# Performance work log

Hardware: AMD Instinct MI355X
Metric: run time of the kernel (lower is better)

The kernel has to match this reference:

```python
import jax, jax.numpy as jnp
import numpy as np

V, B, T, D, H = 32000, 64, 256, 512, 1024


def setup_inputs() -> dict:
    key = jax.random.key(0)
    ks = jax.random.split(key, 8)
    s = lambda i, shape: (jax.random.normal(ks[i], shape, jnp.float32) * 0.02)
    return {
        "y": jax.random.randint(ks[0], (B, T), 0, V),
        "hidden": jnp.zeros((B, H), jnp.float32),
        "emb_table": s(1, (V, D)),
        "Wx": s(2, (D, 3 * H)),
        "Wh": s(3, (H, 3 * H)),
        "bx": jnp.zeros((3 * H,), jnp.float32),
        "bh": jnp.zeros((3 * H,), jnp.float32),
        "W_out": s(4, (H, D)),
        "b_out": jnp.zeros((D,), jnp.float32),
    }


def _gru_step(h, x, Wx, Wh, bx, bh):
    # PyTorch GRUCell semantics: r,z gates, candidate n with r gating the
    # recurrent contribution (including its bias term).
    gx = x @ Wx + bx          # [B, 3H]
    gh = h @ Wh + bh          # [B, 3H]
    xr, xz, xn = jnp.split(gx, 3, axis=-1)
    hr, hz, hn = jnp.split(gh, 3, axis=-1)
    r = jax.nn.sigmoid(xr + hr)
    z = jax.nn.sigmoid(xz + hz)
    n = jnp.tanh(xn + r * hn)
    return (1.0 - z) * n + z * h


def reference(y, hidden, emb_table, Wx, Wh, bx, bh, W_out, b_out):
    emb = emb_table[y]                       # [B, T, D] token embedding lookup

    def step(h, x_t):                        # x_t: [B, D]
        h2 = _gru_step(h, x_t, Wx, Wh, bx, bh)
        return h2, h2

    _, outs = jax.lax.scan(step, hidden, jnp.swapaxes(emb, 0, 1))  # [T, B, H]
    out = jnp.swapaxes(outs, 0, 1)           # [B, T, H] decoder hiddens
    logits = jnp.tanh(out @ W_out + b_out)   # [B, T, D]; dropout_rate=0 -> identity
    return logits
```

## Files before the change

### kernel.cpp

```cpp
#include <hip/hip_runtime.h>
#include <stdint.h>

typedef unsigned short u16;
typedef unsigned int u32;
typedef __attribute__((ext_vector_type(4))) unsigned int u32x4;
typedef __attribute__((ext_vector_type(4))) float f32x4;
typedef __attribute__((ext_vector_type(8))) __bf16 bf16x8;

#define MFMA16(a, b, c) __builtin_amdgcn_mfma_f32_16x16x32_bf16((a), (b), (c), 0, 0, 0)

__device__ __forceinline__ u16 f2b(float f) {
  union { float f; unsigned u; } v; v.f = f;
  unsigned r = v.u + 0x7FFFu + ((v.u >> 16) & 1u);
  return (u16)(r >> 16);
}
__device__ __forceinline__ float b2f(u16 h) {
  union { unsigned u; float f; } v; v.u = ((unsigned)h) << 16;
  return v.f;
}
__device__ __forceinline__ float sigm(float x) { return 1.0f / (1.0f + __expf(-x)); }
__device__ __forceinline__ float tanh_fast(float x) {
  x = fminf(fmaxf(x, -15.0f), 15.0f);
  float t = __expf(2.0f * x);
  return (t - 1.0f) / (t + 1.0f);
}

template <int OFF>
__device__ __forceinline__ u32x4 ld16_sc(const void* p) {
  u32x4 r;
  asm volatile("global_load_dwordx4 %0, %1, off offset:%2 sc0 sc1"
               : "=v"(r) : "v"(p), "i"(OFF));
  return r;
}
__device__ __forceinline__ void st16_sc(void* p, u32x4 v) {
  asm volatile("global_store_dwordx4 %0, %1, off sc0 sc1"
               :: "v"(p), "v"(v) : "memory");
}
__device__ __forceinline__ void st4_sc(u32* p, u32 v) {
  asm volatile("global_store_dword %0, %1, off sc0 sc1"
               :: "v"(p), "v"(v) : "memory");
}
__device__ __forceinline__ u32 ld4_sc(const u32* p) {
  u32 r;
  asm volatile("global_load_dword %0, %1, off sc0 sc1\n\t"
               "s_waitcnt vmcnt(0)"
               : "=v"(r) : "v"(p) : "memory");
  return r;
}

__device__ __forceinline__ void gld_lds16(const void* g, void* l) {
  __builtin_amdgcn_global_load_lds(
      (const __attribute__((address_space(1))) void*)(g),
      (__attribute__((address_space(3))) void*)(l), 16, 0, 0);
}

__global__ __launch_bounds__(256) void prep_all(
    const float* __restrict__ Wx, const float* __restrict__ Wh,
    const float* __restrict__ Wout, const int* __restrict__ y,
    const float* __restrict__ emb, const float* __restrict__ hidden,
    u16* __restrict__ wx_t, u16* __restrict__ wh_t, u16* __restrict__ wo_t,
    u16* __restrict__ aemb, u16* __restrict__ hbuf, u32* __restrict__ tags) {
  __shared__ float tile[32][33];
  const int b = blockIdx.x, tid = threadIdx.x;
  const int tx = tid & 31, ty = tid >> 5;

  const float* src = nullptr; u16* dst = nullptr; int R = 0, C = 0, tb = 0;
  if (b < 1536)      { src = Wx;   dst = wx_t; R = 512;  C = 3072; tb = b; }
  else if (b < 4608) { src = Wh;   dst = wh_t; R = 1024; C = 3072; tb = b - 1536; }
  else if (b < 5120) { src = Wout; dst = wo_t; R = 1024; C = 512;  tb = b - 4608; }

  if (src) {
    const int xt = C >> 5;
    const int c0 = (tb % xt) * 32, r0 = (tb / xt) * 32;
    for (int i = ty; i < 32; i += 8)
      tile[i][tx] = src[(size_t)(r0 + i) * C + (c0 + tx)];
    __syncthreads();
    for (int i = ty; i < 32; i += 8)
      dst[(size_t)(c0 + i) * R + (r0 + tx)] = f2b(tile[tx][i]);
    return;
  }
  if (b < 13312) {
    const int idx = (b - 5120) * 256 + tid;
    const int m = idx >> 7, d0 = (idx & 127) << 2;
    const float4 v = *reinterpret_cast<const float4*>(emb + (size_t)y[m] * 512 + d0);
    ushort4 o;
    o.x = f2b(v.x); o.y = f2b(v.y); o.z = f2b(v.z); o.w = f2b(v.w);
    *reinterpret_cast<ushort4*>(aemb + (size_t)m * 512 + d0) = o;
    return;
  }
  if (b < 13568) {
    const int i = (b - 13312) * 256 + tid;
    const int bb = i >> 10, n = i & 1023;
    const int r = bb >> 4, ii = bb & 15, g = n >> 4, j = n & 15;
    hbuf[((size_t)r * 64 + g) * 256 + ii * 16 + j] = f2b(hidden[(size_t)bb * 1024 + n]);
    return;
  }
  {
    const int base = ((b - 13568) * 256 + tid) * 8;
#pragma unroll
    for (int q = 0; q < 8; ++q) tags[base + q] = 0;
  }
}

template <int EPI, int ALAYOUT>
__global__ __launch_bounds__(256, 2) void gemm_bt(
    const u16* __restrict__ A, const u16* __restrict__ Bt,
    const float* __restrict__ bias, void* __restrict__ Cout,
    int M, int N, int K) {
  __shared__ u16 As[4096], Bs[4096];
  const int tid = threadIdx.x, lane = tid & 63, w = tid >> 6;
  const int wm = w >> 1, wn = w & 1, c = lane & 15, hq = lane >> 4;
  const int m0 = blockIdx.y * 128, n0 = blockIdx.x * 128;
  f32x4 acc[4][4] = {};

  const int r0_ = tid >> 2, ko0 = (tid & 3) << 3;
  const int r1_ = (256 + tid) >> 2, ko1 = ((256 + tid) & 3) << 3;

  for (int k0 = 0; k0 < K; k0 += 32) {
    const u16 *ga0, *ga1;
    if (ALAYOUT == 0) {
      ga0 = A + (size_t)(m0 + r0_) * K + k0 + ko0;
      ga1 = A + (size_t)(m0 + r1_) * K + k0 + ko1;
    } else {
      const int ma = m0 + r0_, ka = k0 + ko0, mb = m0 + r1_, kb = k0 + ko1;
      ga0 = A + ((((size_t)(ma >> 6) + 1) * 4 + ((ma >> 4) & 3)) * 64 +
                 (ka >> 4)) * 256 + (ma & 15) * 16 + (ka & 15);
      ga1 = A + ((((size_t)(mb >> 6) + 1) * 4 + ((mb >> 4) & 3)) * 64 +
                 (kb >> 4)) * 256 + (mb & 15) * 16 + (kb & 15);
    }
    const u16* gb0 = Bt + (size_t)(n0 + r0_) * K + k0 + ko0;
    const u16* gb1 = Bt + (size_t)(n0 + r1_) * K + k0 + ko1;
    __syncthreads();
    gld_lds16(ga0, (char*)As + tid * 16);
    gld_lds16(ga1, (char*)As + 4096 + tid * 16);
    gld_lds16(gb0, (char*)Bs + tid * 16);
    gld_lds16(gb1, (char*)Bs + 4096 + tid * 16);
    __syncthreads();
    u32x4 af[4], bf[4];
#pragma unroll
    for (int i = 0; i < 4; ++i) {
      af[i] = *(const u32x4*)(As + (wm * 64 + i * 16 + c) * 32 + hq * 8);
      bf[i] = *(const u32x4*)(Bs + (wn * 64 + i * 16 + c) * 32 + hq * 8);
    }
#pragma unroll
    for (int mi = 0; mi < 4; ++mi)
#pragma unroll
      for (int ni = 0; ni < 4; ++ni)
        acc[mi][ni] = MFMA16(__builtin_bit_cast(bf16x8, af[mi]),
                             __builtin_bit_cast(bf16x8, bf[ni]), acc[mi][ni]);
  }

#pragma unroll
  for (int ni = 0; ni < 4; ++ni) {
    const int col = n0 + wn * 64 + ni * 16 + c;
    const float bv = bias[col];
#pragma unroll
    for (int mi = 0; mi < 4; ++mi) {
#pragma unroll
      for (int i = 0; i < 4; ++i) {
        const int m = m0 + wm * 64 + mi * 16 + hq * 4 + i;
        const float v = acc[mi][ni][i] + bv;
        if (EPI == 0) {
          const int dr = (m & 255) * 64 + (m >> 8);
          ((u16*)Cout)[(size_t)dr * N + col] = f2b(v);
        } else {
          const int dr = (m & 63) * 256 + (m >> 6);
          ((float*)Cout)[(size_t)dr * N + col] = tanh_fast(v);
        }
      }
    }
  }
}

__global__ __launch_bounds__(320, 1) void scan_kernel(
    const u16* __restrict__ wh_t,
    const float* __restrict__ bh,
    const float* __restrict__ h0,
    const u16* __restrict__ gx,
    u16* __restrict__ hbuf,
    u32* __restrict__ tags) {
  __shared__ u16 whs[96 * 512];
  __shared__ float red[2][4][3][256];
  __shared__ __align__(16) u16 htile[16][16];
  const int g = blockIdx.x >> 2, r = blockIdx.x & 3;
  const int tid = threadIdx.x, lane = tid & 63, s = tid >> 6;
  const int c = lane & 15, hq = lane >> 4;
  const int gcol = g * 16 + c;
  const int row0 = r * 16;

  for (int fb = s; fb < 96; fb += 5) {
    const int ss = fb / 24, kk = (fb % 24) / 3, ct = fb % 3;
    const int n = ct * 1024 + g * 16 + c;
    const int k = ss * 256 + kk * 32 + hq * 8;
    *(u32x4*)(whs + fb * 512 + lane * 8) =
        *(const u32x4*)(wh_t + (size_t)n * 1024 + k);
  }
  float bhv[3], hprev[4];
  u16 gxr[4][3];
  if (s == 4) {
#pragma unroll
    for (int ct = 0; ct < 3; ++ct) bhv[ct] = bh[ct * 1024 + gcol];
#pragma unroll
    for (int i = 0; i < 4; ++i)
      hprev[i] = h0[(size_t)(row0 + hq * 4 + i) * 1024 + gcol];
    const u16* gp = gx + gcol;
#pragma unroll
    for (int i = 0; i < 4; ++i) {
      const int b = row0 + hq * 4 + i;
      gxr[i][0] = gp[(size_t)b * 3072];
      gxr[i][1] = gp[(size_t)b * 3072 + 1024];
      gxr[i][2] = gp[(size_t)b * 3072 + 2048];
    }
  }
  __syncthreads();

  for (int t = 0; t < 256; ++t) {
    if (s < 4) {
      if (t > 0 && lane < 16) {
        const u32* tp = tags + (((size_t)(t & 1) * 4 + r) * 64 + s * 16 + lane) * 32;
        while (__ballot(ld4_sc(tp) < (u32)t)) {}
      }

      u32x4 af[8];
      {
        const u16* ap0 = hbuf + ((size_t)t * 4 + r) * 16384 +
                         (s * 16 + (hq >> 1)) * 256 + c * 16 + (hq & 1) * 8;
        const u16* ap1 = ap0 + 2048;
        af[0] = ld16_sc<0>(ap0);    af[1] = ld16_sc<1024>(ap0);
        af[2] = ld16_sc<2048>(ap0); af[3] = ld16_sc<3072>(ap0);
        af[4] = ld16_sc<0>(ap1);    af[5] = ld16_sc<1024>(ap1);
        af[6] = ld16_sc<2048>(ap1); af[7] = ld16_sc<3072>(ap1);
      }
      asm volatile("s_waitcnt vmcnt(0)" ::: "memory");
      __builtin_amdgcn_sched_barrier(0);

      f32x4 acc[3] = {};
#pragma unroll
      for (int kk = 0; kk < 8; ++kk) {
        const int fb = (s * 8 + kk) * 3;
        const u32x4 b0 = *(const u32x4*)(whs + (fb + 0) * 512 + lane * 8);
        const u32x4 b1 = *(const u32x4*)(whs + (fb + 1) * 512 + lane * 8);
        const u32x4 b2 = *(const u32x4*)(whs + (fb + 2) * 512 + lane * 8);
        const bf16x8 a = __builtin_bit_cast(bf16x8, af[kk]);
        acc[0] = MFMA16(a, __builtin_bit_cast(bf16x8, b0), acc[0]);
        acc[1] = MFMA16(a, __builtin_bit_cast(bf16x8, b1), acc[1]);
        acc[2] = MFMA16(a, __builtin_bit_cast(bf16x8, b2), acc[2]);
      }
#pragma unroll
      for (int ct = 0; ct < 3; ++ct)
        *(f32x4*)&red[t & 1][s][ct][lane * 4] = acc[ct];
    }
    __syncthreads();

    if (s == 4) {
      f32x4 a0 = {}, a1 = {}, a2 = {};
#pragma unroll
      for (int j = 0; j < 4; ++j) {
        a0 += *(const f32x4*)&red[t & 1][j][0][lane * 4];
        a1 += *(const f32x4*)&red[t & 1][j][1][lane * 4];
        a2 += *(const f32x4*)&red[t & 1][j][2][lane * 4];
      }
#pragma unroll
      for (int i = 0; i < 4; ++i) {
        const float xr = b2f(gxr[i][0]);
        const float xz = b2f(gxr[i][1]);
        const float xn = b2f(gxr[i][2]);
        const float rr = sigm(xr + a0[i] + bhv[0]);
        const float zz = sigm(xz + a1[i] + bhv[1]);
        const float nn = tanh_fast(xn + rr * (a2[i] + bhv[2]));
        const float hnew = (1.0f - zz) * nn + zz * hprev[i];
        hprev[i] = hnew;
        htile[hq * 4 + i][c] = f2b(hnew);
      }
      asm volatile("s_waitcnt lgkmcnt(0)" ::: "memory");
      __builtin_amdgcn_sched_barrier(0);
      if (lane < 32) {
        const u32x4 hv = *(const u32x4*)((const u16*)htile + lane * 8);
        st16_sc(hbuf + ((size_t)(t + 1) * 4 + r) * 16384 + g * 256 + lane * 8, hv);
      }
      asm volatile("s_waitcnt vmcnt(0)" ::: "memory");
      if (lane == 0)
        st4_sc(tags + (((size_t)((t + 1) & 1) * 4 + r) * 64 + g) * 32, (u32)(t + 1));
      if (t < 255) {
        const u16* gp = gx + (size_t)(t + 1) * 64 * 3072 + gcol;
#pragma unroll
        for (int i = 0; i < 4; ++i) {
          const int b = row0 + hq * 4 + i;
          gxr[i][0] = gp[(size_t)b * 3072];
          gxr[i][1] = gp[(size_t)b * 3072 + 1024];
          gxr[i][2] = gp[(size_t)b * 3072 + 2048];
        }
      }
    }
  }
}

extern "C" void kernel_launch(void* const* d_in, const int* in_sizes, int n_in,
                              void* d_out, int out_size, void* d_ws, size_t ws_size,
                              hipStream_t stream) {
  (void)in_sizes; (void)n_in; (void)out_size; (void)ws_size;
  const int* y = (const int*)d_in[0];
  const float* hidden = (const float*)d_in[1];
  const float* emb = (const float*)d_in[2];
  const float* Wx = (const float*)d_in[3];
  const float* Wh = (const float*)d_in[4];
  const float* bx = (const float*)d_in[5];
  const float* bh = (const float*)d_in[6];
  const float* Wout = (const float*)d_in[7];
  const float* bout = (const float*)d_in[8];

  char* p = (char*)d_ws;
  u16* wx_t = (u16*)p; p += (size_t)3072 * 512 * 2;
  u16* wh_t = (u16*)p; p += (size_t)3072 * 1024 * 2;
  u16* wo_t = (u16*)p; p += (size_t)512 * 1024 * 2;
  u16* aemb = (u16*)p; p += (size_t)16384 * 512 * 2;
  u16* gx   = (u16*)p; p += (size_t)16384 * 3072 * 2;
  u16* hbuf = (u16*)p; p += (size_t)257 * 4 * 64 * 256 * 2;
  u32* tags = (u32*)p;

  prep_all<<<dim3(13600), dim3(256), 0, stream>>>(Wx, Wh, Wout, y, emb, hidden,
                                                  wx_t, wh_t, wo_t, aemb, hbuf,
                                                  tags);
  gemm_bt<0, 0><<<dim3(24, 128), dim3(256), 0, stream>>>(aemb, wx_t, bx, (void*)gx,
                                                         16384, 3072, 512);
  scan_kernel<<<dim3(256), dim3(320), 0, stream>>>(wh_t, bh, hidden, gx,
                                                   hbuf, tags);
  gemm_bt<1, 1><<<dim3(4, 128), dim3(256), 0, stream>>>(hbuf, wo_t, bout,
                                                        d_out, 16384, 512, 1024);
}
```

Baseline: 876.9 us.

## Replace tag-based inter-block sync with in-band flag bits in hidden-state data

Removes the separate tag array and its store-after-wait handshake. The low mantissa bit of every even bf16 element in the hidden-state buffer now serves as a ready flag. The buffer is zeroed beforehand, consumers poll one element per producer and then re-verify every loaded fragment's flag bits, retrying if any are unset. This cuts a global store, a full vmcnt wait and a separate polling round-trip from each recurrent step's critical path. In exchange it perturbs the LSB of half the hidden values, costs extra zeroing of the whole hbuf in prep, and relies on 16-byte stores becoming visible atomically or on the retry loop covering torn writes.

```diff
diff --git a/kernel.cpp b/kernel.cpp
--- a/kernel.cpp
+++ b/kernel.cpp
@@ -36,17 +36,6 @@
   asm volatile("global_store_dwordx4 %0, %1, off sc0 sc1"
                :: "v"(p), "v"(v) : "memory");
 }
-__device__ __forceinline__ void st4_sc(u32* p, u32 v) {
-  asm volatile("global_store_dword %0, %1, off sc0 sc1"
-               :: "v"(p), "v"(v) : "memory");
-}
-__device__ __forceinline__ u32 ld4_sc(const u32* p) {
-  u32 r;
-  asm volatile("global_load_dword %0, %1, off sc0 sc1\n\t"
-               "s_waitcnt vmcnt(0)"
-               : "=v"(r) : "v"(p) : "memory");
-  return r;
-}
 
 __device__ __forceinline__ void gld_lds16(const void* g, void* l) {
   __builtin_amdgcn_global_load_lds(
@@ -59,7 +48,7 @@
     const float* __restrict__ Wout, const int* __restrict__ y,
     const float* __restrict__ emb, const float* __restrict__ hidden,
     u16* __restrict__ wx_t, u16* __restrict__ wh_t, u16* __restrict__ wo_t,
-    u16* __restrict__ aemb, u16* __restrict__ hbuf, u32* __restrict__ tags) {
+    u16* __restrict__ aemb, u16* __restrict__ hbuf) {
   __shared__ float tile[32][33];
   const int b = blockIdx.x, tid = threadIdx.x;
   const int tx = tid & 31, ty = tid >> 5;
@@ -92,13 +81,15 @@
     const int i = (b - 13312) * 256 + tid;
     const int bb = i >> 10, n = i & 1023;
     const int r = bb >> 4, ii = bb & 15, g = n >> 4, j = n & 15;
-    hbuf[((size_t)r * 64 + g) * 256 + ii * 16 + j] = f2b(hidden[(size_t)bb * 1024 + n]);
+    u16 v = f2b(hidden[(size_t)bb * 1024 + n]);
+    if (!(j & 1)) v |= 1;
+    hbuf[((size_t)r * 64 + g) * 256 + ii * 16 + j] = v;
     return;
   }
   {
-    const int base = ((b - 13568) * 256 + tid) * 8;
-#pragma unroll
-    for (int q = 0; q < 8; ++q) tags[base + q] = 0;
+    const size_t idx = (size_t)(b - 13568) * 256 + tid;
+    u32x4 z = {0, 0, 0, 0};
+    *(u32x4*)(hbuf + 65536 + idx * 8) = z;
   }
 }
 
@@ -177,8 +168,7 @@
     const float* __restrict__ bh,
     const float* __restrict__ h0,
     const u16* __restrict__ gx,
-    u16* __restrict__ hbuf,
-    u32* __restrict__ tags) {
+    u16* __restrict__ hbuf) {
   __shared__ u16 whs[96 * 512];
   __shared__ float red[2][4][3][256];
   __shared__ __align__(16) u16 htile[16][16];
@@ -216,23 +206,42 @@
 
   for (int t = 0; t < 256; ++t) {
     if (s < 4) {
-      if (t > 0 && lane < 16) {
-        const u32* tp = tags + (((size_t)(t & 1) * 4 + r) * 64 + s * 16 + lane) * 32;
-        while (__ballot(ld4_sc(tp) < (u32)t)) {}
+      const u16* slotBase = hbuf + ((size_t)t * 4 + r) * 16384;
+
+      if (t > 0) {
+        const u16* pp = slotBase + (s * 16 + (lane & 15)) * 256;
+        u32 v0, v1;
+        if (lane < 16) {
+          asm volatile("global_load_ushort %0, %1, off sc0 sc1" : "=v"(v0) : "v"(pp));
+          asm volatile("global_load_ushort %0, %1, off sc0 sc1" : "=v"(v1) : "v"(pp));
+          while (true) {
+            asm volatile("s_waitcnt vmcnt(1)" : "+v"(v0));
+            if (!__ballot(!(v0 & 1))) break;
+            asm volatile("global_load_ushort %0, %1, off sc0 sc1" : "=v"(v0) : "v"(pp));
+            asm volatile("s_waitcnt vmcnt(1)" : "+v"(v1));
+            if (!__ballot(!(v1 & 1))) break;
+            asm volatile("global_load_ushort %0, %1, off sc0 sc1" : "=v"(v1) : "v"(pp));
+          }
+        }
       }
 
       u32x4 af[8];
-      {
-        const u16* ap0 = hbuf + ((size_t)t * 4 + r) * 16384 +
-                         (s * 16 + (hq >> 1)) * 256 + c * 16 + (hq & 1) * 8;
-        const u16* ap1 = ap0 + 2048;
+      const u16* ap0 = slotBase + (s * 16 + (hq >> 1)) * 256 + c * 16 + (hq & 1) * 8;
+      const u16* ap1 = ap0 + 2048;
+      while (true) {
         af[0] = ld16_sc<0>(ap0);    af[1] = ld16_sc<1024>(ap0);
         af[2] = ld16_sc<2048>(ap0); af[3] = ld16_sc<3072>(ap0);
         af[4] = ld16_sc<0>(ap1);    af[5] = ld16_sc<1024>(ap1);
         af[6] = ld16_sc<2048>(ap1); af[7] = ld16_sc<3072>(ap1);
-      }
-      asm volatile("s_waitcnt vmcnt(0)" ::: "memory");
-      __builtin_amdgcn_sched_barrier(0);
+        asm volatile("s_waitcnt vmcnt(0)" ::: "memory");
+        __builtin_amdgcn_sched_barrier(0);
+        u32 bad = 0;
+#pragma unroll
+        for (int q = 0; q < 8; ++q)
+#pragma unroll
+          for (int e = 0; e < 4; ++e) bad |= (~af[q][e]) & 1u;
+        if (!__ballot(bad != 0)) break;
+      }
 
       f32x4 acc[3] = {};
 #pragma unroll
@@ -270,7 +279,9 @@
         const float nn = tanh_fast(xn + rr * (a2[i] + bhv[2]));
         const float hnew = (1.0f - zz) * nn + zz * hprev[i];
         hprev[i] = hnew;
-        htile[hq * 4 + i][c] = f2b(hnew);
+        u16 hb = f2b(hnew);
+        if (!(c & 1)) hb |= 1;
+        htile[hq * 4 + i][c] = hb;
       }
       asm volatile("s_waitcnt lgkmcnt(0)" ::: "memory");
       __builtin_amdgcn_sched_barrier(0);
@@ -278,9 +289,6 @@
         const u32x4 hv = *(const u32x4*)((const u16*)htile + lane * 8);
         st16_sc(hbuf + ((size_t)(t + 1) * 4 + r) * 16384 + g * 256 + lane * 8, hv);
       }
-      asm volatile("s_waitcnt vmcnt(0)" ::: "memory");
-      if (lane == 0)
-        st4_sc(tags + (((size_t)((t + 1) & 1) * 4 + r) * 64 + g) * 32, (u32)(t + 1));
       if (t < 255) {
         const u16* gp = gx + (size_t)(t + 1) * 64 * 3072 + gcol;
 #pragma unroll
@@ -316,15 +324,12 @@
   u16* aemb = (u16*)p; p += (size_t)16384 * 512 * 2;
   u16* gx   = (u16*)p; p += (size_t)16384 * 3072 * 2;
   u16* hbuf = (u16*)p; p += (size_t)257 * 4 * 64 * 256 * 2;
-  u32* tags = (u32*)p;
-
-  prep_all<<<dim3(13600), dim3(256), 0, stream>>>(Wx, Wh, Wout, y, emb, hidden,
-                                                  wx_t, wh_t, wo_t, aemb, hbuf,
-                                                  tags);
+
+  prep_all<<<dim3(21760), dim3(256), 0, stream>>>(Wx, Wh, Wout, y, emb, hidden,
+                                                  wx_t, wh_t, wo_t, aemb, hbuf);
   gemm_bt<0, 0><<<dim3(24, 128), dim3(256), 0, stream>>>(aemb, wx_t, bx, (void*)gx,
                                                          16384, 3072, 512);
-  scan_kernel<<<dim3(256), dim3(320), 0, stream>>>(wh_t, bh, hidden, gx,
-                                                   hbuf, tags);
+  scan_kernel<<<dim3(256), dim3(320), 0, stream>>>(wh_t, bh, hidden, gx, hbuf);
   gemm_bt<1, 1><<<dim3(4, 128), dim3(256), 0, stream>>>(hbuf, wo_t, bout,
                                                         d_out, 16384, 512, 1024);
 }
```

Measured after the change: 873.0 us. Within noise of the previous version (-0.4%).
